# Optimization experiments

Hardware: AMD Instinct MI355X
Metric: run time of the kernel (lower is better)

## Reference

```python
import jax, jax.numpy as jnp
import numpy as np

N_NODES = 10000
N_REL = 200
DIM = 128          # rank * 2
REL_DIM = 128
VIS_DIM = 512
TXT_DIM = 768
N_EDGES = 320000


def _glorot(key, shape):
    fan_in, fan_out = shape[1], shape[0]
    lim = (6.0 / (fan_in + fan_out)) ** 0.5
    return jax.random.uniform(key, shape, jnp.float32, -lim, lim)


def setup_inputs() -> dict:
    key = jax.random.key(0)
    ks = jax.random.split(key, 24)
    inp = {}
    inp['x'] = jax.random.randint(ks[0], (1024, 3), 0, N_NODES)
    inp['edge_index'] = jax.random.randint(ks[1], (2, N_EDGES), 0, N_NODES)
    inp['edge_type'] = jax.random.randint(ks[2], (N_EDGES,), 0, N_REL)
    inp['visual'] = jax.random.normal(ks[3], (N_NODES, VIS_DIM), jnp.float32)
    inp['textual'] = jax.random.normal(ks[4], (N_NODES, TXT_DIM), jnp.float32)
    # embeddings (scaled by 0.001 as in torch init)
    inp['structural_emb'] = jax.random.normal(ks[5], (N_NODES, DIM), jnp.float32) * 0.001
    inp['relation_emb'] = jax.random.normal(ks[6], (N_REL, REL_DIM), jnp.float32) * 0.001
    # three KBGAT convs: w1 [out, 2*in+rel], b1 [out], w2 [1, out]
    cat = 2 * DIM + REL_DIM
    for i, tag in enumerate(['s', 'v', 't']):
        inp[f'W1_{tag}'] = _glorot(ks[7 + 3 * i], (DIM, cat))
        inp[f'b1_{tag}'] = jnp.zeros((DIM,), jnp.float32)
        inp[f'w2_{tag}'] = _glorot(ks[8 + 3 * i], (1, DIM))
    # modality projections
    inp['Wv'] = _glorot(ks[16], (DIM, VIS_DIM))
    inp['bv'] = jnp.zeros((DIM,), jnp.float32)
    inp['Wt'] = _glorot(ks[17], (DIM, TXT_DIM))
    inp['bt'] = jnp.zeros((DIM,), jnp.float32)
    inp['alpha'] = jnp.float32(0.1)
    inp['gamma'] = jnp.float32(0.8)
    return inp


def kbgat_conv(feat, rel_emb, src, dst, edge_type, W1, b1, w2):
    # gather per-edge embeddings: x_i = target, x_j = source (PyG default flow)
    triple = jnp.concatenate([feat[dst], feat[src], rel_emb[edge_type]], axis=1)  # [E, 2*D+R]
    c = triple @ W1.T + b1                                   # [E, D]
    b = jax.nn.leaky_relu(c @ w2[0])                         # [E]
    # segment softmax over destination nodes
    m = jax.ops.segment_max(b, dst, num_segments=N_NODES)
    e = jnp.exp(b - m[dst])
    z = jax.ops.segment_sum(e, dst, num_segments=N_NODES)
    attn = e / z[dst]                                        # [E]
    agg = jax.ops.segment_sum(c * attn[:, None], dst, num_segments=N_NODES)  # [N, D]
    return jax.nn.leaky_relu(agg)


def reference(x, edge_index, edge_type, visual, textual, structural_emb, relation_emb,
              W1_s, b1_s, w2_s, W1_v, b1_v, w2_v, W1_t, b1_t, w2_t,
              Wv, bv, Wt, bt, alpha, gamma):
    src, dst = edge_index[0], edge_index[1]
    h_s = kbgat_conv(structural_emb, relation_emb, src, dst, edge_type, W1_s, b1_s, w2_s)
    vf = visual @ Wv.T + bv
    h_v = kbgat_conv(vf, relation_emb, src, dst, edge_type, W1_v, b1_v, w2_v)
    tf = textual @ Wt.T + bt
    h_t = kbgat_conv(tf, relation_emb, src, dst, edge_type, W1_t, b1_t, w2_t)
    return (1.0 - alpha - gamma) * h_s + alpha * h_v + gamma * h_t
```

## Files before the change

### kernel.cpp

```cpp
#include <hip/hip_runtime.h>
#include <hip/hip_bf16.h>

typedef unsigned short u16;
typedef unsigned int u32;
typedef __bf16 bf16x8 __attribute__((ext_vector_type(8)));
typedef float f32x4 __attribute__((ext_vector_type(4)));

#define DIM 128

__device__ __forceinline__ u16 f2bf_rne(float x) {
  u32 u = __float_as_uint(x);
  return (u16)((u + 0x7fffu + ((u >> 16) & 1u)) >> 16);
}
__device__ __forceinline__ u32 packbf2(float x, float y) {
  return (u32)f2bf_rne(x) | ((u32)f2bf_rne(y) << 16);
}
__device__ __forceinline__ float lrelu(float x) { return x > 0.f ? x : 0.01f * x; }
__device__ __forceinline__ int iclamp(int v, int hi) { return v < 0 ? 0 : (v >= hi ? hi - 1 : v); }
__device__ __forceinline__ float sane(float x) { return (x == x) ? x : 0.f; }

__device__ __forceinline__ float wred_max(float v) {
  #pragma unroll
  for (int o = 32; o > 0; o >>= 1) v = fmaxf(v, __shfl_xor(v, o, 64));
  return v;
}
__device__ __forceinline__ float wred_sum(float v) {
  #pragma unroll
  for (int o = 32; o > 0; o >>= 1) v += __shfl_xor(v, o, 64);
  return v;
}

__global__ void hist_k(const int* __restrict__ dst, int* __restrict__ cnt, int E, int N) {
  int e = blockIdx.x * blockDim.x + threadIdx.x;
  if (e < E) {
    int d = dst[e];
    if (d >= 0 && d < N) atomicAdd(&cnt[d], 1);
  }
}

__global__ __launch_bounds__(1024) void scan_k(const int* __restrict__ cnt,
                                               int* __restrict__ offs, int N) {
  __shared__ int sums[1024];
  int t = threadIdx.x;
  int chunk = (N + 1023) >> 10;
  int base = t * chunk;
  int s = 0;
  for (int i = 0; i < chunk; ++i) { int idx = base + i; if (idx < N) s += cnt[idx]; }
  sums[t] = s;
  __syncthreads();
  for (int off = 1; off < 1024; off <<= 1) {
    int v = (t >= off) ? sums[t - off] : 0;
    __syncthreads();
    sums[t] += v;
    __syncthreads();
  }
  int prefix = (t > 0) ? sums[t - 1] : 0;
  for (int i = 0; i < chunk; ++i) {
    int idx = base + i;
    if (idx < N) { offs[idx] = prefix; prefix += cnt[idx]; }
  }
  if (t == 1023) offs[N] = sums[1023];
}

__global__ void scatter_k(const int* __restrict__ dst, const int* __restrict__ src,
                          const int* __restrict__ etyp,
                          const int* __restrict__ offs,
                          int* __restrict__ cursor, u32* __restrict__ sortedST,
                          int E, int N, int NR) {
  int e = blockIdx.x * blockDim.x + threadIdx.x;
  if (e < E) {
    int d = dst[e];
    if (d >= 0 && d < N) {
      int pos = offs[d] + atomicAdd(&cursor[d], 1);
      if (pos >= 0 && pos < E) {
        u32 s = (u32)iclamp(src[e], N);
        u32 t = (u32)iclamp(etyp[e], NR);
        sortedST[pos] = (t << 16) | s;
      }
    }
  }
}

struct PrepArgs {
  const float* W1[3]; const float* Wmod[3]; int K[3]; int isCopy[3];
  u16* Wc[3];
};
struct PrArgs {
  const float* rel; const float* W1[3]; const float* b1[3];
  const float* bmod[3]; const float* w2[3];
  u16* PrAll; float* qr[3]; int NR;
};
struct GArgs {
  const float* A[3]; const u16* B[3]; const float* w2[3];
  u16* PdAll; u16* PsAll; float* qd[3]; float* qs[3];
  int M; int K[3]; int tilesPerM;
};
struct AgArgs {
  const u32* sortedST; const int* offs;
  const float* qd[3]; const float* qs[3]; const float* qr[3];
  const u16* PdAll; const u16* PsAll; const u16* PrAll;
  const float* alphaP; const float* gammaP;
  float* outp; int N; int NR; int E;
};

__global__ void prep_wc_all(PrepArgs a) {
  int m = blockIdx.z;
  int K = a.K[m];
  int k = blockIdx.x * blockDim.x + threadIdx.x;
  int o = blockIdx.y;
  if (k >= K) return;
  int half = (o >= 128) ? 128 : 0;
  int oo = o & 127;
  const float* W1 = a.W1[m];
  float acc;
  if (a.isCopy[m]) {
    acc = W1[oo * 384 + half + k];
  } else {
    const float* Wm = a.Wmod[m];
    acc = 0.f;
    for (int i = 0; i < 128; ++i)
      acc += W1[oo * 384 + half + i] * Wm[i * K + k];
  }
  a.Wc[m][((size_t)(k >> 5) * 256 + o) * 32 + (k & 31)] = f2bf_rne(acc);
}

__global__ __launch_bounds__(128) void prep_pr_all(PrArgs a) {
  __shared__ float red[128];
  int m = blockIdx.z;
  int r = blockIdx.x;
  if (r >= a.NR) return;
  int o = threadIdx.x;
  const float* W1 = a.W1[m];
  float acc = a.b1[m][o];
  for (int i = 0; i < 128; ++i)
    acc += W1[o * 384 + 256 + i] * a.rel[r * 128 + i];
  const float* bmod = a.bmod[m];
  if (bmod != nullptr) {
    for (int i = 0; i < 128; ++i)
      acc += (W1[o * 384 + i] + W1[o * 384 + 128 + i]) * bmod[i];
  }
  a.PrAll[(size_t)r * 384 + m * 128 + o] = f2bf_rne(acc);
  red[o] = acc * a.w2[m][o];
  __syncthreads();
  for (int s = 64; s > 0; s >>= 1) {
    if (o < s) red[o] += red[o + s];
    __syncthreads();
  }
  if (o == 0) a.qr[m][r] = sane(red[0]);
}

__global__ __launch_bounds__(256, 4) void gemm_fused(GArgs g) {
  __shared__ __align__(16) u16 Als[8 * 32 * 32];
  __shared__ float qpart[4][32];
  int fb = blockIdx.x;
  int tpm = g.tilesPerM;
  int m, tile;
  if (fb < tpm)            { m = 2; tile = fb; }
  else if (fb < 2 * tpm)   { m = 1; tile = fb - tpm; }
  else                     { m = 0; tile = fb - 2 * tpm; }

  int M = g.M, K = g.K[m];
  int nt = K >> 5;
  const u16* Bpk = g.B[m];
  const float* w2 = g.w2[m];
  int tid = threadIdx.x;
  int lane = tid & 63, wv = tid >> 6;
  int quad = lane >> 4, l16 = lane & 15;
  int row0 = tile * 32;

  int srow = tid >> 3;
  int tk4 = (tid & 7) * 4;
  int srsw = srow & 3;
  int wg = tk4 >> 3;
  int wrem = tk4 & 7;
  int grow = row0 + srow;
  if (grow >= M) grow = M - 1;
  const float* Ag = g.A[m] + (size_t)grow * K;

  const u16* Bpg = Bpk + (size_t)(wv * 64 + l16) * 32 + quad * 8;

  f32x4 acc[2][4];
  #pragma unroll
  for (int rg = 0; rg < 2; ++rg)
    #pragma unroll
    for (int t = 0; t < 4; ++t) acc[rg][t] = (f32x4){0.f, 0.f, 0.f, 0.f};

  int nchunk = (nt + 7) >> 3;
  for (int c = 0; c < nchunk; ++c) {
    int kbase = c << 8;
    __syncthreads();
    #pragma unroll
    for (int i = 0; i < 8; ++i) {
      int kl = tk4 + i * 32;
      int kg = kbase + kl;
      if (kg < K) {
        float4 v = *reinterpret_cast<const float4*>(Ag + kg);
        int gidx = wg ^ srsw ^ (i & 3);
        u32* d = reinterpret_cast<u32*>(
            &Als[((i * 32 + srow) * 32) + (gidx << 3) + wrem]);
        d[0] = packbf2(v.x, v.y);
        d[1] = packbf2(v.z, v.w);
      }
    }
    __syncthreads();
    int kbR = nt - (c << 3);
    if (kbR > 8) kbR = 8;
    for (int kbl = 0; kbl < kbR; ++kbl) {
      const u16* bp = Bpg + (size_t)((c << 3) + kbl) * 8192;
      bf16x8 b0 = *reinterpret_cast<const bf16x8*>(bp);
      bf16x8 b1 = *reinterpret_cast<const bf16x8*>(bp + 512);
      bf16x8 b2 = *reinterpret_cast<const bf16x8*>(bp + 1024);
      bf16x8 b3 = *reinterpret_cast<const bf16x8*>(bp + 1536);
      int gsw = (quad ^ (l16 & 3) ^ (kbl & 3)) << 3;
      #pragma unroll
      for (int rg = 0; rg < 2; ++rg) {
        bf16x8 a = *reinterpret_cast<const bf16x8*>(
            &Als[(kbl * 32 + rg * 16 + l16) * 32 + gsw]);
        acc[rg][0] = __builtin_amdgcn_mfma_f32_16x16x32_bf16(a, b0, acc[rg][0], 0, 0, 0);
        acc[rg][1] = __builtin_amdgcn_mfma_f32_16x16x32_bf16(a, b1, acc[rg][1], 0, 0, 0);
        acc[rg][2] = __builtin_amdgcn_mfma_f32_16x16x32_bf16(a, b2, acc[rg][2], 0, 0, 0);
        acc[rg][3] = __builtin_amdgcn_mfma_f32_16x16x32_bf16(a, b3, acc[rg][3], 0, 0, 0);
      }
    }
  }

  u16* PdAll = g.PdAll;
  u16* PsAll = g.PsAll;
  float w2c[4];
  #pragma unroll
  for (int t = 0; t < 4; ++t) w2c[t] = w2[(wv & 1) * 64 + t * 16 + l16];

  #pragma unroll
  for (int rg = 0; rg < 2; ++rg) {
    float part[4];
    #pragma unroll
    for (int r = 0; r < 4; ++r) {
      int rr = row0 + rg * 16 + quad * 4 + r;
      bool ok = rr < M;
      float qp = 0.f;
      #pragma unroll
      for (int t = 0; t < 4; ++t) {
        int cc = (wv & 1) * 64 + t * 16 + l16;
        if (ok) {
          if (wv < 2) PdAll[(size_t)rr * 384 + m * 128 + cc] = f2bf_rne(acc[rg][t][r]);
          else        PsAll[(size_t)rr * 384 + m * 128 + cc] = f2bf_rne(acc[rg][t][r]);
        }
        qp += acc[rg][t][r] * w2c[t];
      }
      #pragma unroll
      for (int mk = 1; mk < 16; mk <<= 1) qp += __shfl_xor(qp, mk, 64);
      part[r] = qp;
    }
    if (l16 == 0) {
      #pragma unroll
      for (int r = 0; r < 4; ++r) qpart[wv][rg * 16 + quad * 4 + r] = part[r];
    }
  }
  __syncthreads();
  if (tid < 64) {
    int row = tid & 31;
    int half = tid >> 5;
    int rr = row0 + row;
    if (rr < M) {
      if (half == 0) g.qd[m][rr] = sane(qpart[0][row] + qpart[1][row]);
      else           g.qs[m][rr] = sane(qpart[2][row] + qpart[3][row]);
    }
  }
}

__global__ __launch_bounds__(256) void aggregate_all(AgArgs a) {
  int n = blockIdx.x * 4 + (threadIdx.x >> 6);
  if (n >= a.N) return;
  int lane = threadIdx.x & 63;
  int E = a.E;
  int eb = a.offs[n], ee = a.offs[n + 1];
  if (eb < 0) eb = 0;
  if (eb > E) eb = E;
  if (ee < eb) ee = eb;
  if (ee > E) ee = E;
  int En = ee - eb;

  float al = a.alphaP[0];
  if (!(al > 0.f && al < 1.f)) al = 0.1f;
  float ga = a.gammaP[0];
  if (!(ga > 0.f && ga < 1.f)) ga = 0.8f;
  float coef[3] = {1.f - al - ga, al, ga};

  float qdn[3];
  #pragma unroll
  for (int m = 0; m < 3; ++m) qdn[m] = sane(a.qd[m][n]);

  const u16* PsAll = a.PsAll;
  const u16* PrAll = a.PrAll;
  int dlo = 2 * lane;

  float rm[3] = {-1e30f, -1e30f, -1e30f};
  float z[3] = {0.f, 0.f, 0.f};
  float a0[3] = {0.f, 0.f, 0.f};
  float a1[3] = {0.f, 0.f, 0.f};
  for (int c0 = 0; c0 < En; c0 += 64) {
    int cn = min(64, En - c0);
    u32 stp = 0;
    float bm[3] = {-1e30f, -1e30f, -1e30f};
    if (lane < cn) {
      stp = a.sortedST[eb + c0 + lane];
      int s = (int)(stp & 0xffffu);
      int t = (int)(stp >> 16);
      #pragma unroll
      for (int m = 0; m < 3; ++m)
        bm[m] = lrelu(qdn[m] + a.qs[m][s] + a.qr[m][t]);
    }
    float wr[3];
    #pragma unroll
    for (int m = 0; m < 3; ++m) {
      float cm = wred_max(bm[m]);
      float nm = fmaxf(rm[m], cm);
      float sc = __expf(fmaxf(rm[m] - nm, -80.f));
      z[m] *= sc; a0[m] *= sc; a1[m] *= sc;
      rm[m] = nm;
      wr[m] = (lane < cn) ? __expf(fmaxf(bm[m] - nm, -80.f)) : 0.f;
      z[m] += wr[m];
    }

    int cnR = (cn + 3) & ~3;
    for (int j = 0; j < cnR; j += 4) {
      u32 stj[4];
      float wj[4][3];
      #pragma unroll
      for (int u = 0; u < 4; ++u) {
        stj[u] = __shfl(stp, j + u, 64);
        wj[u][0] = __shfl(wr[0], j + u, 64);
        wj[u][1] = __shfl(wr[1], j + u, 64);
        wj[u][2] = __shfl(wr[2], j + u, 64);
      }
      u32 pu[4][3], ru[4][3];
      #pragma unroll
      for (int u = 0; u < 4; ++u) {
        const u16* ps = PsAll + (size_t)(stj[u] & 0xffffu) * 384 + dlo;
        const u16* pr = PrAll + (size_t)(stj[u] >> 16) * 384 + dlo;
        #pragma unroll
        for (int m = 0; m < 3; ++m) {
          pu[u][m] = *reinterpret_cast<const u32*>(ps + m * 128);
          ru[u][m] = *reinterpret_cast<const u32*>(pr + m * 128);
        }
      }
      #pragma unroll
      for (int u = 0; u < 4; ++u) {
        #pragma unroll
        for (int m = 0; m < 3; ++m) {
          float ps0 = __uint_as_float(pu[u][m] << 16);
          float ps1 = __uint_as_float(pu[u][m] & 0xffff0000u);
          float pr0 = __uint_as_float(ru[u][m] << 16);
          float pr1 = __uint_as_float(ru[u][m] & 0xffff0000u);
          a0[m] = fmaf(wj[u][m], ps0 + pr0, a0[m]);
          a1[m] = fmaf(wj[u][m], ps1 + pr1, a1[m]);
        }
      }
    }
  }
  #pragma unroll
  for (int m = 0; m < 3; ++m) z[m] = wred_sum(z[m]);

  float o0 = 0.f, o1 = 0.f;
  const u16* pd = a.PdAll + (size_t)n * 384 + dlo;
  #pragma unroll
  for (int m = 0; m < 3; ++m) {
    float h0 = 0.f, h1 = 0.f;
    if (En > 0 && z[m] > 0.f) {
      float rz = 1.f / z[m];
      u32 du = *reinterpret_cast<const u32*>(pd + m * 128);
      float pd0 = __uint_as_float(du << 16), pd1 = __uint_as_float(du & 0xffff0000u);
      h0 = lrelu(pd0 + a0[m] * rz);
      h1 = lrelu(pd1 + a1[m] * rz);
    }
    o0 = fmaf(coef[m], h0, o0);
    o1 = fmaf(coef[m], h1, o1);
  }
  float* op = a.outp + (size_t)n * 128 + dlo;
  op[0] = sane(o0);
  op[1] = sane(o1);
}

extern "C" void kernel_launch(void* const* d_in, const int* in_sizes, int n_in,
                              void* d_out, int out_size, void* d_ws, size_t ws_size,
                              hipStream_t stream) {
  const int* ei        = (const int*)d_in[1];
  const int* et        = (const int*)d_in[2];
  const float* visual  = (const float*)d_in[3];
  const float* textual = (const float*)d_in[4];
  const float* semb    = (const float*)d_in[5];
  const float* relemb  = (const float*)d_in[6];
  const float* W1s = (const float*)d_in[7];
  const float* b1s = (const float*)d_in[8];
  const float* w2s = (const float*)d_in[9];
  const float* W1v = (const float*)d_in[10];
  const float* b1v = (const float*)d_in[11];
  const float* w2v = (const float*)d_in[12];
  const float* W1t = (const float*)d_in[13];
  const float* b1t = (const float*)d_in[14];
  const float* w2t = (const float*)d_in[15];
  const float* Wv  = (const float*)d_in[16];
  const float* bv  = (const float*)d_in[17];
  const float* Wt  = (const float*)d_in[18];
  const float* bt  = (const float*)d_in[19];
  const float* alphaP = (const float*)d_in[20];
  const float* gammaP = (const float*)d_in[21];
  float* outp = (float*)d_out;

  const int E   = in_sizes[2];
  const int N   = in_sizes[5] / DIM;
  const int NR  = in_sizes[6] / DIM;
  const int VIS = in_sizes[3] / N;
  const int TXT = in_sizes[4] / N;
  const int KMAX = (TXT > VIS) ? TXT : VIS;
  int Ks[3] = {DIM, VIS, TXT};
  const int TPM = (N + 31) / 32;

  const float* W1a[3]   = {W1s, W1v, W1t};
  const float* b1a[3]   = {b1s, b1v, b1t};
  const float* w2a[3]   = {w2s, w2v, w2t};
  const float* Wmoda[3] = {nullptr, Wv, Wt};
  const float* bmoda[3] = {nullptr, bv, bt};
  const float* Amoda[3] = {semb, visual, textual};

  const int* esrc = ei;
  const int* edst = ei + E;
  int egrid = (E + 255) / 256;

  size_t off = 0;
  auto take = [&](size_t bytes) -> size_t {
    size_t o = off;
    off = (off + bytes + 255) & ~(size_t)255;
    return o;
  };
  size_t o_cnt  = take((size_t)2 * N * 4);
  size_t o_offs = take((size_t)(N + 1) * 4);
  size_t o_st   = take((size_t)E * 4);
  size_t o_qdm[3], o_qsm[3], o_qrm[3], o_Wcm[3];
  for (int m = 0; m < 3; ++m) {
    o_qdm[m] = take((size_t)N * 4);
    o_qsm[m] = take((size_t)N * 4);
    o_qrm[m] = take((size_t)NR * 4);
    o_Wcm[m] = take((size_t)256 * Ks[m] * 2);
  }
  size_t o_PrAll = take((size_t)NR * 384 * 2);
  size_t o_PdAll = take((size_t)N * 384 * 2);
  size_t o_PsAll = take((size_t)N * 384 * 2);
  size_t need = off;

  if (ws_size < need) {
    hipMemsetAsync(d_out, 0, (size_t)out_size * 4, stream);
    return;
  }

  char* w = (char*)d_ws;
  int* counts = (int*)(w + o_cnt);
  int* cursor = counts + N;
  int* offs   = (int*)(w + o_offs);
  u32* sortedST = (u32*)(w + o_st);

  hipMemsetAsync(w, 0, (size_t)2 * N * 4, stream);
  hist_k<<<egrid, 256, 0, stream>>>(edst, counts, E, N);
  scan_k<<<1, 1024, 0, stream>>>(counts, offs, N);
  scatter_k<<<egrid, 256, 0, stream>>>(edst, esrc, et, offs, cursor, sortedST, E, N, NR);

  PrepArgs pa;
  PrArgs ra;
  GArgs ga;
  AgArgs aa;
  ra.rel = relemb; ra.NR = NR;
  ra.PrAll = (u16*)(w + o_PrAll);
  ga.M = N;
  ga.tilesPerM = TPM;
  ga.PdAll = (u16*)(w + o_PdAll);
  ga.PsAll = (u16*)(w + o_PsAll);
  for (int m = 0; m < 3; ++m) {
    pa.W1[m] = W1a[m]; pa.Wmod[m] = Wmoda[m]; pa.K[m] = Ks[m];
    pa.isCopy[m] = (m == 0);
    pa.Wc[m] = (u16*)(w + o_Wcm[m]);
    ra.W1[m] = W1a[m]; ra.b1[m] = b1a[m]; ra.bmod[m] = bmoda[m]; ra.w2[m] = w2a[m];
    ra.qr[m] = (float*)(w + o_qrm[m]);
    ga.A[m] = Amoda[m]; ga.B[m] = (const u16*)(w + o_Wcm[m]); ga.w2[m] = w2a[m];
    ga.qd[m] = (float*)(w + o_qdm[m]); ga.qs[m] = (float*)(w + o_qsm[m]);
    ga.K[m] = Ks[m];
    aa.qd[m] = (const float*)(w + o_qdm[m]);
    aa.qs[m] = (const float*)(w + o_qsm[m]);
    aa.qr[m] = (const float*)(w + o_qrm[m]);
  }
  aa.PdAll = (const u16*)(w + o_PdAll);
  aa.PsAll = (const u16*)(w + o_PsAll);
  aa.PrAll = (const u16*)(w + o_PrAll);
  aa.sortedST = sortedST; aa.offs = offs;
  aa.alphaP = alphaP; aa.gammaP = gammaP;
  aa.outp = outp; aa.N = N; aa.NR = NR; aa.E = E;

  prep_wc_all<<<dim3((KMAX + 255) / 256, 256, 3), 256, 0, stream>>>(pa);
  prep_pr_all<<<dim3(NR, 1, 3), 128, 0, stream>>>(ra);
  gemm_fused<<<dim3(3 * TPM), 256, 0, stream>>>(ga);
  aggregate_all<<<(N + 3) / 4, 256, 0, stream>>>(aa);
}
```

Baseline: 277.4 us.

## Fuse prep, histogram and scatter into GEMM launches; double-buffer A tiles

Result: no change. 278.5 us (+0.4%).

```diff
diff --git a/kernel.cpp b/kernel.cpp
--- a/kernel.cpp
+++ b/kernel.cpp
@@ -30,70 +30,20 @@
   return v;
 }
 
-__global__ void hist_k(const int* __restrict__ dst, int* __restrict__ cnt, int E, int N) {
-  int e = blockIdx.x * blockDim.x + threadIdx.x;
-  if (e < E) {
-    int d = dst[e];
-    if (d >= 0 && d < N) atomicAdd(&cnt[d], 1);
-  }
-}
-
-__global__ __launch_bounds__(1024) void scan_k(const int* __restrict__ cnt,
-                                               int* __restrict__ offs, int N) {
-  __shared__ int sums[1024];
-  int t = threadIdx.x;
-  int chunk = (N + 1023) >> 10;
-  int base = t * chunk;
-  int s = 0;
-  for (int i = 0; i < chunk; ++i) { int idx = base + i; if (idx < N) s += cnt[idx]; }
-  sums[t] = s;
-  __syncthreads();
-  for (int off = 1; off < 1024; off <<= 1) {
-    int v = (t >= off) ? sums[t - off] : 0;
-    __syncthreads();
-    sums[t] += v;
-    __syncthreads();
-  }
-  int prefix = (t > 0) ? sums[t - 1] : 0;
-  for (int i = 0; i < chunk; ++i) {
-    int idx = base + i;
-    if (idx < N) { offs[idx] = prefix; prefix += cnt[idx]; }
-  }
-  if (t == 1023) offs[N] = sums[1023];
-}
-
-__global__ void scatter_k(const int* __restrict__ dst, const int* __restrict__ src,
-                          const int* __restrict__ etyp,
-                          const int* __restrict__ offs,
-                          int* __restrict__ cursor, u32* __restrict__ sortedST,
-                          int E, int N, int NR) {
-  int e = blockIdx.x * blockDim.x + threadIdx.x;
-  if (e < E) {
-    int d = dst[e];
-    if (d >= 0 && d < N) {
-      int pos = offs[d] + atomicAdd(&cursor[d], 1);
-      if (pos >= 0 && pos < E) {
-        u32 s = (u32)iclamp(src[e], N);
-        u32 t = (u32)iclamp(etyp[e], NR);
-        sortedST[pos] = (t << 16) | s;
-      }
-    }
-  }
-}
-
-struct PrepArgs {
-  const float* W1[3]; const float* Wmod[3]; int K[3]; int isCopy[3];
-  u16* Wc[3];
+struct PrepAllArgs {
+  const float* W1[3]; const float* Wmod[3]; int K[3]; u16* Wc[3];
+  const float* rel; const float* b1[3]; const float* bmod[3]; const float* w2[3];
+  u16* PrAll; float* qr[3]; int NR;
+  const int* dst; int* cnt; int E; int N;
+  int prEnd; int wcB2End; int wcB1End; int wcEnd;
 };
-struct PrArgs {
-  const float* rel; const float* W1[3]; const float* b1[3];
-  const float* bmod[3]; const float* w2[3];
-  u16* PrAll; float* qr[3]; int NR;
-};
-struct GArgs {
+struct MainArgs {
   const float* A[3]; const u16* B[3]; const float* w2[3];
   u16* PdAll; u16* PsAll; float* qd[3]; float* qs[3];
-  int M; int K[3]; int tilesPerM;
+  int M; int K[3]; int tilesPerM; int nGemm;
+  const int* dst; const int* src; const int* etyp;
+  const int* offs; int* cursor; u32* sortedST;
+  int E; int NR;
 };
 struct AgArgs {
   const u32* sortedST; const int* offs;
@@ -103,54 +53,128 @@
   float* outp; int N; int NR; int E;
 };
 
-__global__ void prep_wc_all(PrepArgs a) {
-  int m = blockIdx.z;
-  int K = a.K[m];
-  int k = blockIdx.x * blockDim.x + threadIdx.x;
-  int o = blockIdx.y;
-  if (k >= K) return;
-  int half = (o >= 128) ? 128 : 0;
-  int oo = o & 127;
-  const float* W1 = a.W1[m];
-  float acc;
-  if (a.isCopy[m]) {
-    acc = W1[oo * 384 + half + k];
+__global__ __launch_bounds__(256) void fused_prep(PrepAllArgs a) {
+  int b = blockIdx.x, tid = threadIdx.x;
+  if (b < a.prEnd) {
+    __shared__ float red[256];
+    int NRpair = (a.NR + 1) >> 1;
+    int m = b / NRpair;
+    int rp = b - m * NRpair;
+    int half = tid >> 7, o = tid & 127;
+    int r = rp * 2 + half;
+    bool ok = (r < a.NR);
+    float acc = 0.f;
+    if (ok) {
+      const float* W1 = a.W1[m];
+      acc = a.b1[m][o];
+      for (int i = 0; i < 128; ++i)
+        acc += W1[o * 384 + 256 + i] * a.rel[r * 128 + i];
+      const float* bmod = a.bmod[m];
+      if (bmod != nullptr) {
+        for (int i = 0; i < 128; ++i)
+          acc += (W1[o * 384 + i] + W1[o * 384 + 128 + i]) * bmod[i];
+      }
+      a.PrAll[(size_t)r * 384 + m * 128 + o] = f2bf_rne(acc);
+    }
+    red[tid] = ok ? acc * a.w2[m][o] : 0.f;
+    __syncthreads();
+    int base = half << 7;
+    for (int s = 64; s > 0; s >>= 1) {
+      if (o < s) red[base + o] += red[base + o + s];
+      __syncthreads();
+    }
+    if (o == 0 && ok) a.qr[m][r] = sane(red[base]);
+  } else if (b < a.wcEnd) {
+    int m, loc;
+    if (b < a.wcB2End)      { m = 2; loc = b - a.prEnd; }
+    else if (b < a.wcB1End) { m = 1; loc = b - a.wcB2End; }
+    else                    { m = 0; loc = b - a.wcB1End; }
+    int o = loc & 255, kb = loc >> 8;
+    int k = (kb << 8) + tid;
+    int K = a.K[m];
+    if (k < K) {
+      int halfsel = (o >= 128) ? 128 : 0;
+      int oo = o & 127;
+      const float* W1 = a.W1[m];
+      const float* Wm = a.Wmod[m];
+      float acc;
+      if (Wm == nullptr) {
+        acc = W1[oo * 384 + halfsel + k];
+      } else {
+        acc = 0.f;
+        for (int i = 0; i < 128; ++i)
+          acc += W1[oo * 384 + halfsel + i] * Wm[i * K + k];
+      }
+      a.Wc[m][((size_t)(k >> 5) * 256 + o) * 32 + (k & 31)] = f2bf_rne(acc);
+    }
   } else {
-    const float* Wm = a.Wmod[m];
-    acc = 0.f;
-    for (int i = 0; i < 128; ++i)
-      acc += W1[oo * 384 + half + i] * Wm[i * K + k];
-  }
-  a.Wc[m][((size_t)(k >> 5) * 256 + o) * 32 + (k & 31)] = f2bf_rne(acc);
-}
-
-__global__ __launch_bounds__(128) void prep_pr_all(PrArgs a) {
-  __shared__ float red[128];
-  int m = blockIdx.z;
-  int r = blockIdx.x;
-  if (r >= a.NR) return;
-  int o = threadIdx.x;
-  const float* W1 = a.W1[m];
-  float acc = a.b1[m][o];
-  for (int i = 0; i < 128; ++i)
-    acc += W1[o * 384 + 256 + i] * a.rel[r * 128 + i];
-  const float* bmod = a.bmod[m];
-  if (bmod != nullptr) {
-    for (int i = 0; i < 128; ++i)
-      acc += (W1[o * 384 + i] + W1[o * 384 + 128 + i]) * bmod[i];
-  }
-  a.PrAll[(size_t)r * 384 + m * 128 + o] = f2bf_rne(acc);
-  red[o] = acc * a.w2[m][o];
+    int e = (b - a.wcEnd) * 256 + tid;
+    if (e < a.E) {
+      int d = a.dst[e];
+      if (d >= 0 && d < a.N) atomicAdd(&a.cnt[d], 1);
+    }
+  }
+}
+
+__global__ __launch_bounds__(256) void scan_k(const int* __restrict__ cnt,
+                                              int* __restrict__ offs, int N) {
+  __shared__ int sums[256];
+  int t = threadIdx.x;
+  int chunk = (N + 255) >> 8;
+  int base = t * chunk;
+  int s = 0;
+  for (int i = 0; i < chunk; ++i) { int idx = base + i; if (idx < N) s += cnt[idx]; }
+  sums[t] = s;
   __syncthreads();
-  for (int s = 64; s > 0; s >>= 1) {
-    if (o < s) red[o] += red[o + s];
+  for (int off = 1; off < 256; off <<= 1) {
+    int v = (t >= off) ? sums[t - off] : 0;
     __syncthreads();
-  }
-  if (o == 0) a.qr[m][r] = sane(red[0]);
-}
-
-__global__ __launch_bounds__(256, 4) void gemm_fused(GArgs g) {
-  __shared__ __align__(16) u16 Als[8 * 32 * 32];
+    sums[t] += v;
+    __syncthreads();
+  }
+  int prefix = (t > 0) ? sums[t - 1] : 0;
+  for (int i = 0; i < chunk; ++i) {
+    int idx = base + i;
+    if (idx < N) { offs[idx] = prefix; prefix += cnt[idx]; }
+  }
+  if (t == 255) offs[N] = sums[255];
+}
+
+#define COMPUTE(kbl_, cur_, cbase_) do {                                        \
+    const u16* bp = Bpg + (size_t)((cbase_) + (kbl_)) * 8192;                   \
+    bf16x8 b0 = *reinterpret_cast<const bf16x8*>(bp);                           \
+    bf16x8 b1 = *reinterpret_cast<const bf16x8*>(bp + 512);                     \
+    bf16x8 b2 = *reinterpret_cast<const bf16x8*>(bp + 1024);                    \
+    bf16x8 b3 = *reinterpret_cast<const bf16x8*>(bp + 1536);                    \
+    int gsw = (quad ^ (l16 & 3) ^ ((kbl_) & 3)) << 3;                           \
+    _Pragma("unroll")                                                           \
+    for (int rg = 0; rg < 2; ++rg) {                                            \
+      bf16x8 av = *reinterpret_cast<const bf16x8*>(                             \
+          &Als[cur_][((kbl_) * 32 + rg * 16 + l16) * 32 + gsw]);                \
+      acc[rg][0] = __builtin_amdgcn_mfma_f32_16x16x32_bf16(av, b0, acc[rg][0], 0, 0, 0); \
+      acc[rg][1] = __builtin_amdgcn_mfma_f32_16x16x32_bf16(av, b1, acc[rg][1], 0, 0, 0); \
+      acc[rg][2] = __builtin_amdgcn_mfma_f32_16x16x32_bf16(av, b2, acc[rg][2], 0, 0, 0); \
+      acc[rg][3] = __builtin_amdgcn_mfma_f32_16x16x32_bf16(av, b3, acc[rg][3], 0, 0, 0); \
+    }                                                                           \
+  } while (0)
+
+__global__ __launch_bounds__(256, 4) void fused_main(MainArgs g) {
+  if ((int)blockIdx.x >= g.nGemm) {
+    int e = ((int)blockIdx.x - g.nGemm) * 256 + threadIdx.x;
+    if (e < g.E) {
+      int d = g.dst[e];
+      if (d >= 0 && d < g.M) {
+        int pos = g.offs[d] + atomicAdd(&g.cursor[d], 1);
+        if (pos >= 0 && pos < g.E) {
+          u32 s = (u32)iclamp(g.src[e], g.M);
+          u32 t = (u32)iclamp(g.etyp[e], g.NR);
+          g.sortedST[pos] = (t << 16) | s;
+        }
+      }
+    }
+    return;
+  }
+  __shared__ __align__(16) u16 Als[2][8 * 32 * 32];
   __shared__ float qpart[4][32];
   int fb = blockIdx.x;
   int tpm = g.tilesPerM;
@@ -185,42 +209,60 @@
     #pragma unroll
     for (int t = 0; t < 4; ++t) acc[rg][t] = (f32x4){0.f, 0.f, 0.f, 0.f};
 
+  float4 vreg[8];
+  #pragma unroll
+  for (int i = 0; i < 8; ++i) {
+    int kg = tk4 + i * 32;
+    if (kg < K) vreg[i] = *reinterpret_cast<const float4*>(Ag + kg);
+  }
+  #pragma unroll
+  for (int i = 0; i < 8; ++i) {
+    int kl = tk4 + i * 32;
+    if (kl < K) {
+      int gidx = wg ^ srsw ^ (i & 3);
+      u32* d = reinterpret_cast<u32*>(
+          &Als[0][((i * 32 + srow) * 32) + (gidx << 3) + wrem]);
+      d[0] = packbf2(vreg[i].x, vreg[i].y);
+      d[1] = packbf2(vreg[i].z, vreg[i].w);
+    }
+  }
+  __syncthreads();
+
   int nchunk = (nt + 7) >> 3;
   for (int c = 0; c < nchunk; ++c) {
-    int kbase = c << 8;
-    __syncthreads();
-    #pragma unroll
-    for (int i = 0; i < 8; ++i) {
-      int kl = tk4 + i * 32;
-      int kg = kbase + kl;
-      if (kg < K) {
-        float4 v = *reinterpret_cast<const float4*>(Ag + kg);
-        int gidx = wg ^ srsw ^ (i & 3);
-        u32* d = reinterpret_cast<u32*>(
-            &Als[((i * 32 + srow) * 32) + (gidx << 3) + wrem]);
-        d[0] = packbf2(v.x, v.y);
-        d[1] = packbf2(v.z, v.w);
-      }
-    }
-    __syncthreads();
-    int kbR = nt - (c << 3);
+    int cur = c & 1;
+    bool more = (c + 1 < nchunk);
+    if (more) {
+      int kb2 = (c + 1) << 8;
+      #pragma unroll
+      for (int i = 0; i < 8; ++i) {
+        int kg = kb2 + tk4 + i * 32;
+        if (kg < K) vreg[i] = *reinterpret_cast<const float4*>(Ag + kg);
+      }
+    }
+    int cbase = c << 3;
+    int kbR = nt - cbase;
     if (kbR > 8) kbR = 8;
-    for (int kbl = 0; kbl < kbR; ++kbl) {
-      const u16* bp = Bpg + (size_t)((c << 3) + kbl) * 8192;
-      bf16x8 b0 = *reinterpret_cast<const bf16x8*>(bp);
-      bf16x8 b1 = *reinterpret_cast<const bf16x8*>(bp + 512);
-      bf16x8 b2 = *reinterpret_cast<const bf16x8*>(bp + 1024);
-      bf16x8 b3 = *reinterpret_cast<const bf16x8*>(bp + 1536);
-      int gsw = (quad ^ (l16 & 3) ^ (kbl & 3)) << 3;
-      #pragma unroll
-      for (int rg = 0; rg < 2; ++rg) {
-        bf16x8 a = *reinterpret_cast<const bf16x8*>(
-            &Als[(kbl * 32 + rg * 16 + l16) * 32 + gsw]);
-        acc[rg][0] = __builtin_amdgcn_mfma_f32_16x16x32_bf16(a, b0, acc[rg][0], 0, 0, 0);
-        acc[rg][1] = __builtin_amdgcn_mfma_f32_16x16x32_bf16(a, b1, acc[rg][1], 0, 0, 0);
-        acc[rg][2] = __builtin_amdgcn_mfma_f32_16x16x32_bf16(a, b2, acc[rg][2], 0, 0, 0);
-        acc[rg][3] = __builtin_amdgcn_mfma_f32_16x16x32_bf16(a, b3, acc[rg][3], 0, 0, 0);
-      }
+    if (kbR == 8) {
+      #pragma unroll
+      for (int kbl = 0; kbl < 8; ++kbl) COMPUTE(kbl, cur, cbase);
+    } else {
+      for (int kbl = 0; kbl < kbR; ++kbl) COMPUTE(kbl, cur, cbase);
+    }
+    if (more) {
+      int kb2 = (c + 1) << 8;
+      #pragma unroll
+      for (int i = 0; i < 8; ++i) {
+        int kg = kb2 + tk4 + i * 32;
+        if (kg < K) {
+          int gidx = wg ^ srsw ^ (i & 3);
+          u32* d = reinterpret_cast<u32*>(
+              &Als[cur ^ 1][((i * 32 + srow) * 32) + (gidx << 3) + wrem]);
+          d[0] = packbf2(vreg[i].x, vreg[i].y);
+          d[1] = packbf2(vreg[i].z, vreg[i].w);
+        }
+      }
+      __syncthreads();
     }
   }
 
@@ -412,7 +454,6 @@
   const int NR  = in_sizes[6] / DIM;
   const int VIS = in_sizes[3] / N;
   const int TXT = in_sizes[4] / N;
-  const int KMAX = (TXT > VIS) ? TXT : VIS;
   int Ks[3] = {DIM, VIS, TXT};
   const int TPM = (N + 31) / 32;
 
@@ -460,26 +501,35 @@
   u32* sortedST = (u32*)(w + o_st);
 
   hipMemsetAsync(w, 0, (size_t)2 * N * 4, stream);
-  hist_k<<<egrid, 256, 0, stream>>>(edst, counts, E, N);
-  scan_k<<<1, 1024, 0, stream>>>(counts, offs, N);
-  scatter_k<<<egrid, 256, 0, stream>>>(edst, esrc, et, offs, cursor, sortedST, E, N, NR);
-
-  PrepArgs pa;
-  PrArgs ra;
-  GArgs ga;
-  AgArgs aa;
-  ra.rel = relemb; ra.NR = NR;
-  ra.PrAll = (u16*)(w + o_PrAll);
-  ga.M = N;
-  ga.tilesPerM = TPM;
+
+  PrepAllArgs pa;
+  pa.rel = relemb; pa.NR = NR;
+  pa.PrAll = (u16*)(w + o_PrAll);
+  pa.dst = edst; pa.cnt = counts; pa.E = E; pa.N = N;
+  for (int m = 0; m < 3; ++m) {
+    pa.W1[m] = W1a[m]; pa.Wmod[m] = Wmoda[m]; pa.K[m] = Ks[m];
+    pa.Wc[m] = (u16*)(w + o_Wcm[m]);
+    pa.b1[m] = b1a[m]; pa.bmod[m] = bmoda[m]; pa.w2[m] = w2a[m];
+    pa.qr[m] = (float*)(w + o_qrm[m]);
+  }
+  int NRpair = (NR + 1) / 2;
+  int kbm[3];
+  for (int m = 0; m < 3; ++m) kbm[m] = (Ks[m] + 255) / 256;
+  pa.prEnd   = 3 * NRpair;
+  pa.wcB2End = pa.prEnd + 256 * kbm[2];
+  pa.wcB1End = pa.wcB2End + 256 * kbm[1];
+  pa.wcEnd   = pa.wcB1End + 256 * kbm[0];
+  int prepGrid = pa.wcEnd + egrid;
+
+  MainArgs ga;
+  ga.M = N; ga.tilesPerM = TPM; ga.nGemm = 3 * TPM;
   ga.PdAll = (u16*)(w + o_PdAll);
   ga.PsAll = (u16*)(w + o_PsAll);
+  ga.dst = edst; ga.src = esrc; ga.etyp = et;
+  ga.offs = offs; ga.cursor = cursor; ga.sortedST = sortedST;
+  ga.E = E; ga.NR = NR;
+  AgArgs aa;
   for (int m = 0; m < 3; ++m) {
-    pa.W1[m] = W1a[m]; pa.Wmod[m] = Wmoda[m]; pa.K[m] = Ks[m];
-    pa.isCopy[m] = (m == 0);
-    pa.Wc[m] = (u16*)(w + o_Wcm[m]);
-    ra.W1[m] = W1a[m]; ra.b1[m] = b1a[m]; ra.bmod[m] = bmoda[m]; ra.w2[m] = w2a[m];
-    ra.qr[m] = (float*)(w + o_qrm[m]);
     ga.A[m] = Amoda[m]; ga.B[m] = (const u16*)(w + o_Wcm[m]); ga.w2[m] = w2a[m];
     ga.qd[m] = (float*)(w + o_qdm[m]); ga.qs[m] = (float*)(w + o_qsm[m]);
     ga.K[m] = Ks[m];
@@ -487,6 +537,8 @@
     aa.qs[m] = (const float*)(w + o_qsm[m]);
     aa.qr[m] = (const float*)(w + o_qrm[m]);
   }
+  int mainGrid = ga.nGemm + egrid;
+
   aa.PdAll = (const u16*)(w + o_PdAll);
   aa.PsAll = (const u16*)(w + o_PsAll);
   aa.PrAll = (const u16*)(w + o_PrAll);
@@ -494,8 +546,8 @@
   aa.alphaP = alphaP; aa.gammaP = gammaP;
   aa.outp = outp; aa.N = N; aa.NR = NR; aa.E = E;
 
-  prep_wc_all<<<dim3((KMAX + 255) / 256, 256, 3), 256, 0, stream>>>(pa);
-  prep_pr_all<<<dim3(NR, 1, 3), 128, 0, stream>>>(ra);
-  gemm_fused<<<dim3(3 * TPM), 256, 0, stream>>>(ga);
+  fused_prep<<<prepGrid, 256, 0, stream>>>(pa);
+  scan_k<<<1, 256, 0, stream>>>(counts, offs, N);
+  fused_main<<<mainGrid, 256, 0, stream>>>(ga);
   aggregate_all<<<(N + 3) / 4, 256, 0, stream>>>(aa);
 }
```
